# Optimization experiments

Measured on AMD Instinct MI355X. Metric: run time of the kernel, lower is better.

Reference implementation:

```python
import jax, jax.numpy as jnp
import numpy as np

DIM = 768
NUM_HEADS = 12
HEAD_DIM = DIM // NUM_HEADS
B, N = 16, 784


def setup_inputs() -> dict:
    key = jax.random.key(0)
    k1, k2, k3, k4, k5 = jax.random.split(key, 5)
    x = jax.random.normal(k1, (B, N, DIM), dtype=jnp.float32)
    # Dense params (flax Dense: kernel [in, out], bias [out])
    Wqkv = jax.random.normal(k2, (DIM, 3 * DIM), dtype=jnp.float32) * (DIM ** -0.5)
    bqkv = jnp.zeros((3 * DIM,), dtype=jnp.float32)
    Wo = jax.random.normal(k3, (DIM, DIM), dtype=jnp.float32) * (DIM ** -0.5)
    bo = jnp.zeros((DIM,), dtype=jnp.float32)
    return {"x": x, "Wqkv": Wqkv, "bqkv": bqkv, "Wo": Wo, "bo": bo}


def reference(x, Wqkv, bqkv, Wo, bo):
    b, n, dim = x.shape
    # fused QKV projection
    qkv = jnp.einsum('bnd,df->bnf', x, Wqkv) + bqkv          # [b, n, 3*dim]
    qkv = qkv.reshape(b, n, 3, NUM_HEADS, HEAD_DIM)           # '(k h d)' split
    q, k, v = qkv[:, :, 0], qkv[:, :, 1], qkv[:, :, 2]        # [b, n, h, d]
    scale = HEAD_DIM ** -0.5
    # chunked/flash path computes exact softmax attention; same math, expressed densely
    scores = jnp.einsum('bihd,bjhd->bhij', q, k) * scale      # [b, h, n, n]
    attn = jax.nn.softmax(scores, axis=-1)
    out = jnp.einsum('bhij,bjhd->bihd', attn, v)              # [b, n, h, d]
    out = out.reshape(b, n, dim)                              # 'b n (h d)'
    return jnp.einsum('bnd,df->bnf', out, Wo) + bo
```

## Files before the change

kernel.cpp:

```cpp
#include <hip/hip_runtime.h>

#define DIM 768
#define NHEADS 12
#define HDIM 64
#define BB 16
#define NN 784
#define M_TOTAL (BB * NN)

typedef __attribute__((ext_vector_type(8))) _Float16 f16x8;
typedef __attribute__((ext_vector_type(4))) float f32x4;
typedef __attribute__((ext_vector_type(16))) float f32x16;

typedef __attribute__((address_space(3))) unsigned int lds_uint;
typedef __attribute__((address_space(1))) const unsigned int g_uint;
__device__ inline void gload_lds16(const void* g, void* l) {
    __builtin_amdgcn_global_load_lds((g_uint*)(uintptr_t)g,
                                     (lds_uint*)(uintptr_t)l, 16, 0, 0);
}

__global__ __launch_bounds__(256) void cvt_f16_kernel(
    const float* __restrict__ in, _Float16* __restrict__ out, int n)
{
    int i = (blockIdx.x * 256 + threadIdx.x) * 8;
    if (i >= n) return;
    float4 a = *(const float4*)&in[i];
    float4 b = *(const float4*)&in[i + 4];
    union { _Float16 h[8]; uint4 v; } o;
    o.h[0] = (_Float16)a.x; o.h[1] = (_Float16)a.y;
    o.h[2] = (_Float16)a.z; o.h[3] = (_Float16)a.w;
    o.h[4] = (_Float16)b.x; o.h[5] = (_Float16)b.y;
    o.h[6] = (_Float16)b.z; o.h[7] = (_Float16)b.w;
    *(uint4*)&out[i] = o.v;
}

__global__ __launch_bounds__(256) void transpose_f16_kernel(
    const float* __restrict__ W, _Float16* __restrict__ T, int K, int N)
{
    __shared__ float t[32][33];
    const int n0 = blockIdx.x * 32, k0 = blockIdx.y * 32;
    const int r = threadIdx.x >> 3, c4 = (threadIdx.x & 7) * 4;
    float4 v = *(const float4*)&W[(size_t)(k0 + r) * N + n0 + c4];
    t[r][c4 + 0] = v.x; t[r][c4 + 1] = v.y;
    t[r][c4 + 2] = v.z; t[r][c4 + 3] = v.w;
    __syncthreads();
    union { _Float16 h[4]; ushort4 v4; } o;
#pragma unroll
    for (int i = 0; i < 4; ++i) o.h[i] = (_Float16)t[c4 + i][r];
    *(ushort4*)&T[(size_t)(n0 + r) * K + k0 + c4] = o.v4;
}

template <int OUT_F16>
__global__ __launch_bounds__(256) void gemm_f16_kernel(
    const _Float16* __restrict__ A, const _Float16* __restrict__ B,
    const float* __restrict__ bias, void* __restrict__ Cout,
    int M, int N, int K)
{
    __shared__ _Float16 sA[128 * 64];
    __shared__ _Float16 sB[128 * 64];

    const int tid  = threadIdx.x;
    const int wave = tid >> 6;
    const int lane = tid & 63;
    const int gm = blockIdx.y * 128;
    const int gn = blockIdx.x * 128;
    const int wm = (wave & 1) * 64;
    const int wn = (wave >> 1) * 64;
    const int l31 = lane & 31;
    const int hi  = lane >> 5;

    const int srow = lane >> 3;
    const int scol = (((lane & 7) ^ (srow & 7)) * 8);

    f32x16 acc[2][2] = {};

    for (int k0 = 0; k0 < K; k0 += 64) {
        __syncthreads();
#pragma unroll
        for (int i = 0; i < 4; ++i) {
            const int rbase = wave * 32 + i * 8;
            gload_lds16(A + (size_t)(gm + rbase + srow) * K + k0 + scol,
                        &sA[rbase * 64]);
            gload_lds16(B + (size_t)(gn + rbase + srow) * K + k0 + scol,
                        &sB[rbase * 64]);
        }
        __syncthreads();

#pragma unroll
        for (int kk = 0; kk < 4; ++kk) {
            const int c = kk * 2 + hi;
            const int sw = (c ^ (l31 & 7)) * 8;
            f16x8 a[2], bf[2];
#pragma unroll
            for (int mt = 0; mt < 2; ++mt)
                a[mt] = *(const f16x8*)&sA[(wm + mt * 32 + l31) * 64 + sw];
#pragma unroll
            for (int nt = 0; nt < 2; ++nt)
                bf[nt] = *(const f16x8*)&sB[(wn + nt * 32 + l31) * 64 + sw];
#pragma unroll
            for (int mt = 0; mt < 2; ++mt)
#pragma unroll
                for (int nt = 0; nt < 2; ++nt)
                    acc[mt][nt] = __builtin_amdgcn_mfma_f32_32x32x16_f16(
                        a[mt], bf[nt], acc[mt][nt], 0, 0, 0);
        }
    }

#pragma unroll
    for (int nt = 0; nt < 2; ++nt) {
        const int col = gn + wn + nt * 32 + l31;
        const float bv = bias[col];
#pragma unroll
        for (int mt = 0; mt < 2; ++mt) {
            f32x16 v = acc[mt][nt];
#pragma unroll
            for (int reg = 0; reg < 16; ++reg) {
                const int row = gm + wm + mt * 32 + (reg & 3) + 8 * (reg >> 2) + 4 * hi;
                const float o = v[reg] + bv;
                if (OUT_F16)
                    ((_Float16*)Cout)[(size_t)row * N + col] = (_Float16)o;
                else
                    ((float*)Cout)[(size_t)row * N + col] = o;
            }
        }
    }
}

#define LOG2E_8 0.18033688f

#define ATTN_TILE(J0, TAIL)                                                    \
  {                                                                            \
    const int j0_ = (J0);                                                      \
    int jrowK = j0_ + sj;                                                      \
    if (TAIL && jrowK > NN - 1) jrowK = NN - 1;                                \
    const size_t kbase = (size_t)(b * NN + jrowK) * (3 * DIM) + DIM + h * HDIM;\
    uint4 k0v = *(const uint4*)&qkv[kbase + sg * 8];                           \
    uint4 k1v = *(const uint4*)&qkv[kbase + sg * 8 + 32];                      \
    int vr0 = j0_ + 2 * jj, vr1 = j0_ + 2 * jj + 1;                            \
    if (TAIL) { if (vr0 > NN - 1) vr0 = NN - 1; if (vr1 > NN - 1) vr1 = NN - 1; } \
    const size_t vb0 = (size_t)(b * NN + vr0) * (3 * DIM) + 2 * DIM + h * HDIM + dsub; \
    const size_t vb1 = (size_t)(b * NN + vr1) * (3 * DIM) + 2 * DIM + h * HDIM + dsub; \
    union { uint4 v; _Float16 h[8]; } va, vc;                                  \
    va.v = *(const uint4*)&qkv[vb0];                                           \
    vc.v = *(const uint4*)&qkv[vb1];                                           \
    __syncthreads();                                                           \
    *(uint4*)&Ks[sj][sg * 8]      = k0v;                                       \
    *(uint4*)&Ks[sj][sg * 8 + 32] = k1v;                                       \
    _Pragma("unroll")                                                          \
    for (int i = 0; i < 8; ++i) {                                              \
        union { _Float16 h[2]; unsigned int u; } t;                            \
        t.h[0] = va.h[i]; t.h[1] = vc.h[i];                                    \
        *(unsigned int*)&Vt[dsub + i][pcol] = t.u;                             \
    }                                                                          \
    __syncthreads();                                                           \
    f32x4 s[4] = {};                                                           \
    _Pragma("unroll")                                                          \
    for (int nt = 0; nt < 4; ++nt) {                                           \
        f16x8 kf0 = *(const f16x8*)&Ks[nt * 16 + l16][quad * 8];               \
        f16x8 kf1 = *(const f16x8*)&Ks[nt * 16 + l16][32 + quad * 8];          \
        s[nt] = __builtin_amdgcn_mfma_f32_16x16x32_f16(kf0, qfrag[0], s[nt], 0, 0, 0); \
        s[nt] = __builtin_amdgcn_mfma_f32_16x16x32_f16(kf1, qfrag[1], s[nt], 0, 0, 0); \
    }                                                                          \
    unsigned int pk[4][2];                                                     \
    _Pragma("unroll")                                                          \
    for (int nt = 0; nt < 4; ++nt) {                                           \
        float pv[4];                                                           \
        _Pragma("unroll")                                                      \
        for (int r = 0; r < 4; ++r) {                                          \
            float p = exp2f(s[nt][r]);                                         \
            if (TAIL && (j0_ + nt * 16) >= NN) p = 0.f;                        \
            lpart += p;                                                        \
            pv[r] = p;                                                         \
        }                                                                      \
        union { _Float16 h[2]; unsigned int u; } c0, c1;                       \
        c0.h[0] = (_Float16)pv[0]; c0.h[1] = (_Float16)pv[1];                  \
        c1.h[0] = (_Float16)pv[2]; c1.h[1] = (_Float16)pv[3];                  \
        pk[nt][0] = c0.u; pk[nt][1] = c1.u;                                    \
    }                                                                          \
    _Pragma("unroll")                                                          \
    for (int pc = 0; pc < 2; ++pc) {                                           \
        union { unsigned int u[4]; f16x8 v; } pa;                              \
        pa.u[0] = pk[2 * pc][0];     pa.u[1] = pk[2 * pc][1];                  \
        pa.u[2] = pk[2 * pc + 1][0]; pa.u[3] = pk[2 * pc + 1][1];              \
        _Pragma("unroll")                                                      \
        for (int dt = 0; dt < 4; ++dt) {                                       \
            f16x8 vf = *(const f16x8*)&Vt[dt * 16 + l16][pc * 32 + quad * 8];  \
            O[dt] = __builtin_amdgcn_mfma_f32_16x16x32_f16(pa.v, vf, O[dt], 0, 0, 0); \
        }                                                                      \
    }                                                                          \
  }

__global__ __launch_bounds__(256) void attn_f16_kernel(
    const _Float16* __restrict__ qkv, _Float16* __restrict__ oat)
{
    const int L   = blockIdx.x + 13 * (blockIdx.y + NHEADS * blockIdx.z);
    const int xcd = L & 7, ixc = L >> 3;
    const int grp = xcd * 24 + ixc / 13;
    const int q0  = (ixc % 13) * 64;
    const int b   = grp / NHEADS;
    const int h   = grp % NHEADS;

    const int tid = threadIdx.x;
    const int wave = tid >> 6;
    const int lane = tid & 63;
    const int quad = lane >> 4;
    const int l16  = lane & 15;

    __shared__ _Float16 Ks[64][72];
    __shared__ _Float16 Vt[64][72];

    f16x8 qfrag[2];
    {
        int qrow = q0 + wave * 16 + l16; if (qrow > NN - 1) qrow = NN - 1;
        size_t base = (size_t)(b * NN + qrow) * (3 * DIM) + h * HDIM;
        f16x8 q0v = *(const f16x8*)&qkv[base + quad * 8];
        f16x8 q1v = *(const f16x8*)&qkv[base + 32 + quad * 8];
        qfrag[0] = q0v * (_Float16)LOG2E_8;
        qfrag[1] = q1v * (_Float16)LOG2E_8;
    }

    const int sj = lane;
    const int sg = wave;
    const int jj   = lane & 31;
    const int dsub = sg * 16 + (lane >> 5) * 8;
    const int pcol = ((jj >> 4) << 5) | (((jj >> 1) & 3) << 3)
                   | (((jj >> 3) & 1) << 2) | ((jj & 1) << 1);

    f32x4 O[4] = {};
    float lpart = 0.f;

    for (int jt = 0; jt < 12; ++jt) {
        ATTN_TILE(jt * 64, 0)
    }
    ATTN_TILE(768, 1)

    float t = lpart;
    t += __shfl_xor(t, 16);
    t += __shfl_xor(t, 32);
    float inv[4];
#pragma unroll
    for (int r = 0; r < 4; ++r)
        inv[r] = 1.0f / __shfl(t, quad * 4 + r, 16);

#pragma unroll
    for (int r = 0; r < 4; ++r) {
        const int q = q0 + wave * 16 + quad * 4 + r;
        if (q < NN) {
#pragma unroll
            for (int dt = 0; dt < 4; ++dt) {
                const size_t base = (size_t)(b * NN + q) * DIM + h * HDIM + dt * 16 + l16;
                oat[base] = (_Float16)(O[dt][r] * inv[r]);
            }
        }
    }
}

extern "C" void kernel_launch(void* const* d_in, const int* in_sizes, int n_in,
                              void* d_out, int out_size, void* d_ws, size_t ws_size,
                              hipStream_t stream) {
    const float* x    = (const float*)d_in[0];
    const float* Wqkv = (const float*)d_in[1];
    const float* bqkv = (const float*)d_in[2];
    const float* Wo   = (const float*)d_in[3];
    const float* bo   = (const float*)d_in[4];
    float* out = (float*)d_out;

    _Float16* qkv = (_Float16*)d_ws;
    _Float16* xh  = qkv + (size_t)M_TOTAL * 3 * DIM;
    _Float16* wqT = xh + (size_t)M_TOTAL * DIM;
    _Float16* woT = wqT + (size_t)3 * DIM * DIM;
    _Float16* oat = xh;

    {
        int n = M_TOTAL * DIM;
        cvt_f16_kernel<<<n / 8 / 256, 256, 0, stream>>>(x, xh, n);
    }
    transpose_f16_kernel<<<dim3((3 * DIM) / 32, DIM / 32), 256, 0, stream>>>(
        Wqkv, wqT, DIM, 3 * DIM);
    transpose_f16_kernel<<<dim3(DIM / 32, DIM / 32), 256, 0, stream>>>(
        Wo, woT, DIM, DIM);
    gemm_f16_kernel<1><<<dim3((3 * DIM) / 128, M_TOTAL / 128), 256, 0, stream>>>(
        xh, wqT, bqkv, qkv, M_TOTAL, 3 * DIM, DIM);
    attn_f16_kernel<<<dim3(13, NHEADS, BB), 256, 0, stream>>>(qkv, oat);
    gemm_f16_kernel<0><<<dim3(DIM / 128, M_TOTAL / 128), 256, 0, stream>>>(
        oat, woT, bo, out, M_TOTAL, DIM, DIM);
}
```

Baseline: 265.3 us.

## Double query tile per attention block, prefetch K/V, and XCD-remap GEMM blocks

```diff
diff --git a/kernel.cpp b/kernel.cpp
--- a/kernel.cpp
+++ b/kernel.cpp
@@ -61,8 +61,15 @@
     const int tid  = threadIdx.x;
     const int wave = tid >> 6;
     const int lane = tid & 63;
-    const int gm = blockIdx.y * 128;
-    const int gn = blockIdx.x * 128;
+
+    const int nwg = gridDim.x * gridDim.y;
+    const int lid = blockIdx.x + gridDim.x * blockIdx.y;
+    const int cq  = nwg >> 3, cr = nwg & 7;
+    const int xcd = lid & 7, ix = lid >> 3;
+    const int wgid = (xcd < cr ? xcd * (cq + 1) : cr * (cq + 1) + (xcd - cr) * cq) + ix;
+    const int gn = (wgid % gridDim.x) * 128;
+    const int gm = (wgid / gridDim.x) * 128;
+
     const int wm = (wave & 1) * 64;
     const int wn = (wave >> 1) * 64;
     const int l31 = lane & 31;
@@ -127,75 +134,84 @@
 
 #define LOG2E_8 0.18033688f
 
-#define ATTN_TILE(J0, TAIL)                                                    \
+#define LOAD_TILE(J0, TAIL)                                                    \
   {                                                                            \
     const int j0_ = (J0);                                                      \
     int jrowK = j0_ + sj;                                                      \
     if (TAIL && jrowK > NN - 1) jrowK = NN - 1;                                \
     const size_t kbase = (size_t)(b * NN + jrowK) * (3 * DIM) + DIM + h * HDIM;\
-    uint4 k0v = *(const uint4*)&qkv[kbase + sg * 8];                           \
-    uint4 k1v = *(const uint4*)&qkv[kbase + sg * 8 + 32];                      \
+    k0v = *(const uint4*)&qkv[kbase + sg * 8];                                 \
+    k1v = *(const uint4*)&qkv[kbase + sg * 8 + 32];                            \
     int vr0 = j0_ + 2 * jj, vr1 = j0_ + 2 * jj + 1;                            \
     if (TAIL) { if (vr0 > NN - 1) vr0 = NN - 1; if (vr1 > NN - 1) vr1 = NN - 1; } \
-    const size_t vb0 = (size_t)(b * NN + vr0) * (3 * DIM) + 2 * DIM + h * HDIM + dsub; \
-    const size_t vb1 = (size_t)(b * NN + vr1) * (3 * DIM) + 2 * DIM + h * HDIM + dsub; \
-    union { uint4 v; _Float16 h[8]; } va, vc;                                  \
-    va.v = *(const uint4*)&qkv[vb0];                                           \
-    vc.v = *(const uint4*)&qkv[vb1];                                           \
-    __syncthreads();                                                           \
+    va.v = *(const uint4*)&qkv[(size_t)(b * NN + vr0) * (3 * DIM) + 2 * DIM + h * HDIM + dsub]; \
+    vc.v = *(const uint4*)&qkv[(size_t)(b * NN + vr1) * (3 * DIM) + 2 * DIM + h * HDIM + dsub]; \
+  }
+
+#define WRITE_TILE()                                                           \
+  {                                                                            \
     *(uint4*)&Ks[sj][sg * 8]      = k0v;                                       \
     *(uint4*)&Ks[sj][sg * 8 + 32] = k1v;                                       \
     _Pragma("unroll")                                                          \
     for (int i = 0; i < 8; ++i) {                                              \
-        union { _Float16 h[2]; unsigned int u; } t;                            \
-        t.h[0] = va.h[i]; t.h[1] = vc.h[i];                                    \
+        union { _Float16 h2[2]; unsigned int u; } t;                           \
+        t.h2[0] = va.h[i]; t.h2[1] = vc.h[i];                                  \
         *(unsigned int*)&Vt[dsub + i][pcol] = t.u;                             \
     }                                                                          \
-    __syncthreads();                                                           \
-    f32x4 s[4] = {};                                                           \
+  }
+
+#define EXP_PACK(SV, G, J0_, TAIL)                                             \
+  {                                                                            \
+    float p0 = exp2f(SV[0]), p1 = exp2f(SV[1]);                                \
+    float p2 = exp2f(SV[2]), p3 = exp2f(SV[3]);                                \
+    if (TAIL && (J0_ + nt * 16) >= NN) { p0 = p1 = p2 = p3 = 0.f; }            \
+    lpart[G] += (p0 + p1) + (p2 + p3);                                         \
+    union { _Float16 h2[2]; unsigned int u; } c0, c1;                          \
+    c0.h2[0] = (_Float16)p0; c0.h2[1] = (_Float16)p1;                          \
+    c1.h2[0] = (_Float16)p2; c1.h2[1] = (_Float16)p3;                          \
+    pk[G][nt][0] = c0.u; pk[G][nt][1] = c1.u;                                  \
+  }
+
+#define COMPUTE_TILE(J0, TAIL)                                                 \
+  {                                                                            \
+    unsigned int pk[2][4][2];                                                  \
     _Pragma("unroll")                                                          \
     for (int nt = 0; nt < 4; ++nt) {                                           \
         f16x8 kf0 = *(const f16x8*)&Ks[nt * 16 + l16][quad * 8];               \
         f16x8 kf1 = *(const f16x8*)&Ks[nt * 16 + l16][32 + quad * 8];          \
-        s[nt] = __builtin_amdgcn_mfma_f32_16x16x32_f16(kf0, qfrag[0], s[nt], 0, 0, 0); \
-        s[nt] = __builtin_amdgcn_mfma_f32_16x16x32_f16(kf1, qfrag[1], s[nt], 0, 0, 0); \
+        f32x4 s0 = {}, s1 = {};                                                \
+        s0 = __builtin_amdgcn_mfma_f32_16x16x32_f16(kf0, qfrag[0][0], s0, 0, 0, 0); \
+        s0 = __builtin_amdgcn_mfma_f32_16x16x32_f16(kf1, qfrag[0][1], s0, 0, 0, 0); \
+        s1 = __builtin_amdgcn_mfma_f32_16x16x32_f16(kf0, qfrag[1][0], s1, 0, 0, 0); \
+        s1 = __builtin_amdgcn_mfma_f32_16x16x32_f16(kf1, qfrag[1][1], s1, 0, 0, 0); \
+        EXP_PACK(s0, 0, J0, TAIL)                                              \
+        EXP_PACK(s1, 1, J0, TAIL)                                              \
     }                                                                          \
-    unsigned int pk[4][2];                                                     \
-    _Pragma("unroll")                                                          \
-    for (int nt = 0; nt < 4; ++nt) {                                           \
-        float pv[4];                                                           \
-        _Pragma("unroll")                                                      \
-        for (int r = 0; r < 4; ++r) {                                          \
-            float p = exp2f(s[nt][r]);                                         \
-            if (TAIL && (j0_ + nt * 16) >= NN) p = 0.f;                        \
-            lpart += p;                                                        \
-            pv[r] = p;                                                         \
-        }                                                                      \
-        union { _Float16 h[2]; unsigned int u; } c0, c1;                       \
-        c0.h[0] = (_Float16)pv[0]; c0.h[1] = (_Float16)pv[1];                  \
-        c1.h[0] = (_Float16)pv[2]; c1.h[1] = (_Float16)pv[3];                  \
-        pk[nt][0] = c0.u; pk[nt][1] = c1.u;                                    \
-    }                                                                          \
+    __builtin_amdgcn_s_setprio(1);                                             \
     _Pragma("unroll")                                                          \
     for (int pc = 0; pc < 2; ++pc) {                                           \
-        union { unsigned int u[4]; f16x8 v; } pa;                              \
-        pa.u[0] = pk[2 * pc][0];     pa.u[1] = pk[2 * pc][1];                  \
-        pa.u[2] = pk[2 * pc + 1][0]; pa.u[3] = pk[2 * pc + 1][1];              \
+        union { unsigned int u[4]; f16x8 v; } pa0, pa1;                        \
+        pa0.u[0] = pk[0][2 * pc][0];     pa0.u[1] = pk[0][2 * pc][1];          \
+        pa0.u[2] = pk[0][2 * pc + 1][0]; pa0.u[3] = pk[0][2 * pc + 1][1];      \
+        pa1.u[0] = pk[1][2 * pc][0];     pa1.u[1] = pk[1][2 * pc][1];          \
+        pa1.u[2] = pk[1][2 * pc + 1][0]; pa1.u[3] = pk[1][2 * pc + 1][1];      \
         _Pragma("unroll")                                                      \
         for (int dt = 0; dt < 4; ++dt) {                                       \
             f16x8 vf = *(const f16x8*)&Vt[dt * 16 + l16][pc * 32 + quad * 8];  \
-            O[dt] = __builtin_amdgcn_mfma_f32_16x16x32_f16(pa.v, vf, O[dt], 0, 0, 0); \
+            O[0][dt] = __builtin_amdgcn_mfma_f32_16x16x32_f16(pa0.v, vf, O[0][dt], 0, 0, 0); \
+            O[1][dt] = __builtin_amdgcn_mfma_f32_16x16x32_f16(pa1.v, vf, O[1][dt], 0, 0, 0); \
         }                                                                      \
     }                                                                          \
+    __builtin_amdgcn_s_setprio(0);                                             \
   }
 
-__global__ __launch_bounds__(256) void attn_f16_kernel(
+__global__ __launch_bounds__(256, 4) void attn_f16_kernel(
     const _Float16* __restrict__ qkv, _Float16* __restrict__ oat)
 {
-    const int L   = blockIdx.x + 13 * (blockIdx.y + NHEADS * blockIdx.z);
+    const int L   = blockIdx.x + 7 * (blockIdx.y + NHEADS * blockIdx.z);
     const int xcd = L & 7, ixc = L >> 3;
-    const int grp = xcd * 24 + ixc / 13;
-    const int q0  = (ixc % 13) * 64;
+    const int grp = xcd * 24 + ixc / 7;
+    const int q0  = (ixc % 7) * 128;
     const int b   = grp / NHEADS;
     const int h   = grp % NHEADS;
 
@@ -208,14 +224,13 @@
     __shared__ _Float16 Ks[64][72];
     __shared__ _Float16 Vt[64][72];
 
-    f16x8 qfrag[2];
-    {
-        int qrow = q0 + wave * 16 + l16; if (qrow > NN - 1) qrow = NN - 1;
+    f16x8 qfrag[2][2];
+#pragma unroll
+    for (int g = 0; g < 2; ++g) {
+        int qrow = q0 + wave * 32 + g * 16 + l16; if (qrow > NN - 1) qrow = NN - 1;
         size_t base = (size_t)(b * NN + qrow) * (3 * DIM) + h * HDIM;
-        f16x8 q0v = *(const f16x8*)&qkv[base + quad * 8];
-        f16x8 q1v = *(const f16x8*)&qkv[base + 32 + quad * 8];
-        qfrag[0] = q0v * (_Float16)LOG2E_8;
-        qfrag[1] = q1v * (_Float16)LOG2E_8;
+        qfrag[g][0] = (*(const f16x8*)&qkv[base + quad * 8]) * (_Float16)LOG2E_8;
+        qfrag[g][1] = (*(const f16x8*)&qkv[base + 32 + quad * 8]) * (_Float16)LOG2E_8;
     }
 
     const int sj = lane;
@@ -225,30 +240,49 @@
     const int pcol = ((jj >> 4) << 5) | (((jj >> 1) & 3) << 3)
                    | (((jj >> 3) & 1) << 2) | ((jj & 1) << 1);
 
-    f32x4 O[4] = {};
-    float lpart = 0.f;
-
-    for (int jt = 0; jt < 12; ++jt) {
-        ATTN_TILE(jt * 64, 0)
-    }
-    ATTN_TILE(768, 1)
-
-    float t = lpart;
-    t += __shfl_xor(t, 16);
-    t += __shfl_xor(t, 32);
-    float inv[4];
-#pragma unroll
-    for (int r = 0; r < 4; ++r)
-        inv[r] = 1.0f / __shfl(t, quad * 4 + r, 16);
-
-#pragma unroll
-    for (int r = 0; r < 4; ++r) {
-        const int q = q0 + wave * 16 + quad * 4 + r;
-        if (q < NN) {
-#pragma unroll
-            for (int dt = 0; dt < 4; ++dt) {
-                const size_t base = (size_t)(b * NN + q) * DIM + h * HDIM + dt * 16 + l16;
-                oat[base] = (_Float16)(O[dt][r] * inv[r]);
+    f32x4 O[2][4] = {};
+    float lpart[2] = {0.f, 0.f};
+
+    uint4 k0v, k1v;
+    union { uint4 v; _Float16 h[8]; } va, vc;
+
+    LOAD_TILE(0, 0)
+#pragma unroll 1
+    for (int jt = 0; jt < 11; ++jt) {
+        __syncthreads();
+        WRITE_TILE()
+        __syncthreads();
+        LOAD_TILE((jt + 1) * 64, 0)
+        COMPUTE_TILE(0, 0)
+    }
+    __syncthreads();
+    WRITE_TILE()
+    __syncthreads();
+    LOAD_TILE(768, 1)
+    COMPUTE_TILE(704, 0)
+    __syncthreads();
+    WRITE_TILE()
+    __syncthreads();
+    COMPUTE_TILE(768, 1)
+
+#pragma unroll
+    for (int g = 0; g < 2; ++g) {
+        float t = lpart[g];
+        t += __shfl_xor(t, 16);
+        t += __shfl_xor(t, 32);
+        float inv[4];
+#pragma unroll
+        for (int r = 0; r < 4; ++r)
+            inv[r] = 1.0f / __shfl(t, quad * 4 + r, 16);
+#pragma unroll
+        for (int r = 0; r < 4; ++r) {
+            const int q = q0 + wave * 32 + g * 16 + quad * 4 + r;
+            if (q < NN) {
+#pragma unroll
+                for (int dt = 0; dt < 4; ++dt) {
+                    const size_t base = (size_t)(b * NN + q) * DIM + h * HDIM + dt * 16 + l16;
+                    oat[base] = (_Float16)(O[g][dt][r] * inv[r]);
+                }
             }
         }
     }
@@ -280,7 +314,7 @@
         Wo, woT, DIM, DIM);
     gemm_f16_kernel<1><<<dim3((3 * DIM) / 128, M_TOTAL / 128), 256, 0, stream>>>(
         xh, wqT, bqkv, qkv, M_TOTAL, 3 * DIM, DIM);
-    attn_f16_kernel<<<dim3(13, NHEADS, BB), 256, 0, stream>>>(qkv, oat);
+    attn_f16_kernel<<<dim3(7, NHEADS, BB), 256, 0, stream>>>(qkv, oat);
     gemm_f16_kernel<0><<<dim3(DIM / 128, M_TOTAL / 128), 256, 0, stream>>>(
         oat, woT, bo, out, M_TOTAL, DIM, DIM);
 }
```

Result: slower. 282.9 us (+6.6%).
